# Optimization experiments

Hardware: AMD Instinct MI355X
Metric: run time of the kernel (lower is better)

## Reference

```python
import jax, jax.numpy as jnp
import numpy as np

MU = 255.0
WINDOW, STRIDE = 16, 8
N_LAYERS, R = 16, 64
LOOP_FACTOR = 8  # floor(log2(max_dilation=128)) + 1


def mu_law_encode(x):
    x = jnp.clip(x, -1.0, 1.0)
    m = jnp.sign(x) * jnp.log1p(MU * jnp.abs(x)) / jnp.log1p(MU)
    return jnp.clip((m + 1.0) * 0.5 * MU + 0.5, 0, MU).astype(jnp.int32)


def conv_transpose1d(x, w, b, stride):
    # torch ConvTranspose1d semantics, weight [Cin, Cout, K], padding=0
    K = w.shape[-1]
    rhs = jnp.transpose(jnp.flip(w, -1), (1, 0, 2))  # -> [Cout, Cin, K]
    y = jax.lax.conv_general_dilated(
        x, rhs, window_strides=(1,), padding=[(K - 1, K - 1)],
        lhs_dilation=(stride,), dimension_numbers=('NCH', 'OIH', 'NCH'))
    return y + b[None, :, None]


def causal_conv(x, w, b, dilation):
    # left-pad by (K-1)*dilation, then valid dilated conv (torch Conv1d weight [O,I,K])
    K = w.shape[-1]
    xp = jnp.pad(x, ((0, 0), (0, 0), ((K - 1) * dilation, 0)))
    y = jax.lax.conv_general_dilated(
        xp, w, window_strides=(1,), padding='VALID',
        rhs_dilation=(dilation,), dimension_numbers=('NCH', 'OIH', 'NCH'))
    return y + b[None, :, None]


def pconv(x, w, b=None):
    # 1x1 conv as matmul over channel dim
    y = jnp.einsum('oc,bct->bot', w, x)
    return y if b is None else y + b[None, :, None]


def wavenet_fwd(features, audio_q, w_up, b_up, w_cond, b_cond, embed,
                w_dil, b_dil, w_res, b_res, w_skip, b_skip, w_out, w_end):
    B, T = audio_q.shape
    cond = conv_transpose1d(features, w_up, b_up, STRIDE)
    pad = WINDOW - STRIDE  # fading == 'full'
    cond = cond[..., pad:-pad]
    cond = pconv(cond, w_cond, b_cond)        # applied inside get_cond_input
    cond = cond[..., :T]
    cond_acts = pconv(cond, w_cond, b_cond)   # applied AGAIN in forward (as in source)
    cond_acts = cond_acts.reshape(B, N_LAYERS, 2 * R, T)
    x = jnp.swapaxes(embed[audio_q], 1, 2)    # [B, R, T]
    output = None
    res_acts = None
    for i in range(N_LAYERS):
        d = 2 ** (i % LOOP_FACTOR)
        ia = causal_conv(x, w_dil[i], b_dil[i], d) + cond_acts[:, i]
        acts = jnp.tanh(ia[:, :R]) * jax.nn.sigmoid(ia[:, R:])
        if i < N_LAYERS - 1:
            res_acts = pconv(acts, w_res[i], b_res[i])
        x = res_acts + x  # last layer reuses previous res_acts (faithful to source)
        skip = pconv(acts, w_skip[i], b_skip[i])
        output = skip if i == 0 else output + skip
    out = jax.nn.relu(output)
    out = jax.nn.relu(pconv(out, w_out))      # conv_out, no bias
    out = pconv(out, w_end)                   # conv_end, no bias
    # shift right by one, first frame zeroed
    out = jnp.concatenate([jnp.zeros_like(out[:, :, :1]), out[:, :, :-1]], axis=2)
    return out


def setup_inputs() -> dict:
    key = jax.random.key(0)
    ks = jax.random.split(key, 16)
    f32 = jnp.float32
    return {
        'features': jax.random.normal(ks[0], (1, 2048, 128), f32),
        'audio': jax.random.uniform(ks[1], (1, 1016), f32, -1.0, 1.0),
        'w_up': jax.random.normal(ks[2], (2048, 2048, 16), f32) * 0.01,
        'b_up': jax.random.normal(ks[3], (2048,), f32) * 0.01,
        'w_cond': jax.random.normal(ks[4], (2048, 2048), f32) * 0.02,
        'b_cond': jax.random.normal(ks[5], (2048,), f32) * 0.02,
        'embed': jax.random.normal(ks[6], (256, 64), f32) * 0.1,
        'w_dil': jax.random.normal(ks[7], (16, 128, 64, 2), f32) * 0.1,
        'b_dil': jax.random.normal(ks[8], (16, 128), f32) * 0.02,
        'w_res': jax.random.normal(ks[9], (15, 64, 64), f32) * 0.1,
        'b_res': jax.random.normal(ks[10], (15, 64), f32) * 0.02,
        'w_skip': jax.random.normal(ks[11], (16, 256, 64), f32) * 0.1,
        'b_skip': jax.random.normal(ks[12], (16, 256), f32) * 0.02,
        'w_out': jax.random.normal(ks[13], (256, 256), f32) * 0.05,
        'w_end': jax.random.normal(ks[14], (256, 256), f32) * 0.05,
    }


def reference(features, audio, w_up, b_up, w_cond, b_cond, embed,
              w_dil, b_dil, w_res, b_res, w_skip, b_skip, w_out, w_end):
    q = mu_law_encode(audio)
    out = wavenet_fwd(features, q, w_up, b_up, w_cond, b_cond, embed,
                      w_dil, b_dil, w_res, b_res, w_skip, b_skip, w_out, w_end)
    return (out, q)
```

## Files before the change

kernel.cpp:

```cpp
#include <hip/hip_runtime.h>
#include <math.h>

#define T_LEN 1016

typedef __attribute__((ext_vector_type(8))) short bf16x8;
typedef __attribute__((ext_vector_type(4))) float f32x4;
typedef __attribute__((ext_vector_type(4))) unsigned int uint4v;
typedef __attribute__((ext_vector_type(2))) unsigned int uint2v;

static __device__ __forceinline__ unsigned pk_bf16(float lo, float hi) {
    unsigned r;
    asm("v_cvt_pk_bf16_f32 %0, %1, %2" : "=v"(r) : "v"(lo), "v"(hi));
    return r;
}

#define F4C(v, i) ((i) == 0 ? (v).x : (i) == 1 ? (v).y : (i) == 2 ? (v).z : (v).w)

__global__ void k_mulaw_embed(const float* __restrict__ audio,
                              const float* __restrict__ embed,
                              float* __restrict__ x0,
                              float* __restrict__ q_out)
{
    int t = blockIdx.x * blockDim.x + threadIdx.x;
    if (t >= T_LEN) return;
    float x = audio[t];
    x = fminf(1.f, fmaxf(-1.f, x));
    float ax = fabsf(x);
    float sg = (x > 0.f) ? 1.f : ((x < 0.f) ? -1.f : 0.f);
    float m = sg * log1pf(255.f * ax) / log1pf(255.f);
    float v = (m + 1.f) * 0.5f * 255.f + 0.5f;
    v = fminf(255.f, fmaxf(0.f, v));
    int q = (int)v;
    q_out[t] = (float)q;
    const float* e = embed + q * 64;
    for (int c = 0; c < 64; ++c) x0[(size_t)c * T_LEN + t] = e[c];
}

__global__ __launch_bounds__(256) void k_cvt_bf16(const float* __restrict__ src,
                                                  unsigned short* __restrict__ dst)
{
    int i4 = (blockIdx.x * 256 + threadIdx.x) * 4;
    float4 v = *(const float4*)&src[i4];
    uint2v p;
    p.x = pk_bf16(v.x, v.y);
    p.y = pk_bf16(v.z, v.w);
    *(uint2v*)&dst[i4] = p;
}

__global__ __launch_bounds__(256) void k_build_f2t(const float* __restrict__ F,
                                                   unsigned short* __restrict__ f2t)
{
    int oct = blockIdx.x;
    for (int c = threadIdx.x; c < 2048; c += 256) {
        float v0 = (oct < 127) ? F[(size_t)c * 128 + oct] : 0.f;
        float v1 = (oct < 127) ? F[(size_t)c * 128 + oct + 1] : 0.f;
        *(unsigned*)&f2t[(size_t)oct * 4096 + 2 * c] = pk_bf16(v0, v1);
    }
}

__global__ __launch_bounds__(256) void k_upsample_mfma(
    const unsigned short* __restrict__ f2t,
    const float* __restrict__ W,
    const float* __restrict__ b_up,
    unsigned short* __restrict__ cond0)
{
    __shared__ char lds_raw[49152];

    const int tid  = threadIdx.x;
    const int wave = tid >> 6;
    const int lane = tid & 63;
    const int ob   = blockIdx.x * 8;
    const int wm = wave & 1, wn = wave >> 1;
    const int row = lane & 15, g = lane >> 4;

    int cj[2], wbyte[2][4];
    size_t aWoff[2];
    #pragma unroll
    for (int j = 0; j < 2; ++j) {
        int flat = j * 256 + tid;
        int cp = flat >> 4;
        int op = (flat >> 1) & 7;
        int h  = flat & 1;
        cj[j] = cp;
        aWoff[j] = (size_t)cp * 32768 + (size_t)(ob + op) * 16 + h * 4;
        #pragma unroll
        for (int i = 0; i < 4; ++i) {
            int ph = h * 4 + i;
            int m  = op * 8 + ph;
            wbyte[j][i] = m * 128 + ((cp * 4) ^ (ph << 4));
        }
    }
    const int bn = tid >> 1, bhalf = tid & 1;
    int bSrc[4], bbw[4];
    #pragma unroll
    for (int q = 0; q < 4; ++q) {
        bSrc[q] = bn * 4096 + bhalf * 32 + q * 8;
        bbw[q]  = bn * 128 + ((((bhalf * 4 + q) * 16)) ^ ((bn & 7) << 4));
    }
    int abyte[2][2], bbyte[2][4];
    #pragma unroll
    for (int s = 0; s < 2; ++s) {
        #pragma unroll
        for (int fm = 0; fm < 2; ++fm) {
            int m = wm * 32 + fm * 16 + row;
            abyte[s][fm] = m * 128 + (((s * 4 + g) * 16) ^ ((m & 7) << 4));
        }
        #pragma unroll
        for (int fn = 0; fn < 4; ++fn) {
            int n = wn * 64 + fn * 16 + row;
            bbyte[s][fn] = n * 128 + (((s * 4 + g) * 16) ^ ((n & 7) << 4));
        }
    }

    f32x4 acc[2][4];
    #pragma unroll
    for (int a = 0; a < 2; ++a)
        #pragma unroll
        for (int b = 0; b < 4; ++b) acc[a][b] = (f32x4){0.f, 0.f, 0.f, 0.f};

    float4 aL[2], aH[2];
    uint4v bstg[4];

    #pragma unroll
    for (int j = 0; j < 2; ++j) {
        const float* p = W + aWoff[j];
        aL[j] = *(const float4*)p;
        aH[j] = *(const float4*)(p + 8);
    }
    #pragma unroll
    for (int q = 0; q < 4; ++q)
        bstg[q] = *(const uint4v*)(f2t + bSrc[q]);
    #pragma unroll
    for (int j = 0; j < 2; ++j)
        #pragma unroll
        for (int i = 0; i < 4; ++i)
            *(unsigned*)(lds_raw + wbyte[j][i]) = pk_bf16(F4C(aH[j], i), F4C(aL[j], i));
    #pragma unroll
    for (int q = 0; q < 4; ++q)
        *(uint4v*)(lds_raw + 16384 + bbw[q]) = bstg[q];
    __syncthreads();

    int cur = 0;
    for (int r = 0; r < 64; ++r) {
        const bool more = (r < 63);
        if (more) {
            const size_t roff = (size_t)(r + 1) * (32 * 32768);
            #pragma unroll
            for (int j = 0; j < 2; ++j) {
                const float* p = W + aWoff[j] + roff;
                aL[j] = *(const float4*)p;
                aH[j] = *(const float4*)(p + 8);
            }
            const int bo = (r + 1) * 64;
            #pragma unroll
            for (int q = 0; q < 4; ++q)
                bstg[q] = *(const uint4v*)(f2t + bSrc[q] + bo);
        }
        {
            const char* As = lds_raw + cur * 8192;
            const char* Bs = lds_raw + 16384 + cur * 16384;
            #pragma unroll
            for (int s = 0; s < 2; ++s) {
                bf16x8 af[2];
                #pragma unroll
                for (int fm = 0; fm < 2; ++fm)
                    af[fm] = *(const bf16x8*)(As + abyte[s][fm]);
                #pragma unroll
                for (int fn = 0; fn < 4; ++fn) {
                    bf16x8 bf = *(const bf16x8*)(Bs + bbyte[s][fn]);
                    acc[0][fn] = __builtin_amdgcn_mfma_f32_16x16x32_bf16(af[0], bf, acc[0][fn], 0, 0, 0);
                    acc[1][fn] = __builtin_amdgcn_mfma_f32_16x16x32_bf16(af[1], bf, acc[1][fn], 0, 0, 0);
                }
            }
        }
        if (more) {
            char* As = lds_raw + (cur ^ 1) * 8192;
            char* Bs = lds_raw + 16384 + (cur ^ 1) * 16384;
            #pragma unroll
            for (int j = 0; j < 2; ++j)
                #pragma unroll
                for (int i = 0; i < 4; ++i)
                    *(unsigned*)(As + wbyte[j][i]) = pk_bf16(F4C(aH[j], i), F4C(aL[j], i));
            #pragma unroll
            for (int q = 0; q < 4; ++q)
                *(uint4v*)(Bs + bbw[q]) = bstg[q];
        }
        __syncthreads();
        cur ^= 1;
    }

    #pragma unroll
    for (int fm = 0; fm < 2; ++fm) {
        const int och = ob + wm * 4 + fm * 2 + (g >> 1);
        const int ph0 = (g & 1) * 4;
        const float bb = b_up[och];
        #pragma unroll
        for (int fn = 0; fn < 4; ++fn) {
            const int oct = wn * 64 + fn * 16 + row;
            if (oct == 127) continue;
            float v0 = acc[fm][fn].x + bb;
            float v1 = acc[fm][fn].y + bb;
            float v2 = acc[fm][fn].z + bb;
            float v3 = acc[fm][fn].w + bb;
            uint2v pkd;
            pkd.x = pk_bf16(v0, v1);
            pkd.y = pk_bf16(v2, v3);
            *(uint2v*)&cond0[(size_t)och * 1024 + oct * 8 + ph0] = pkd;
        }
    }
}

__global__ __launch_bounds__(256) void k_transpose_bf16(const unsigned short* __restrict__ src,
                                                        unsigned short* __restrict__ dst)
{
    __shared__ unsigned short sm[64][68];
    const int t0 = blockIdx.x * 64, o0 = blockIdx.y * 64;
    const int tid = threadIdx.x;
    const int r = tid >> 4;
    const int c4 = (tid & 15) * 4;
    #pragma unroll
    for (int p = 0; p < 4; ++p) {
        int o = p * 16 + r;
        ushort4 v = *(const ushort4*)(src + (size_t)(o0 + o) * 1024 + t0 + c4);
        sm[o][c4 + 0] = v.x; sm[o][c4 + 1] = v.y;
        sm[o][c4 + 2] = v.z; sm[o][c4 + 3] = v.w;
    }
    __syncthreads();
    #pragma unroll
    for (int p = 0; p < 4; ++p) {
        int t = p * 16 + r;
        int tg = t0 + t;
        ushort4 v;
        if (tg < 1016) {
            v.x = sm[c4 + 0][t]; v.y = sm[c4 + 1][t];
            v.z = sm[c4 + 2][t]; v.w = sm[c4 + 3][t];
        } else {
            v.x = 0; v.y = 0; v.z = 0; v.w = 0;
        }
        *(ushort4*)(dst + (size_t)tg * 2048 + o0 + c4) = v;
    }
}

template<int MODE>
__global__ __launch_bounds__(256) void gemm_mfma(
    const unsigned short* __restrict__ A, const unsigned short* __restrict__ Bm,
    const float* __restrict__ bias, void* __restrict__ outp,
    int ldA, int ldB, int K)
{
    const int w = threadIdx.x >> 6, lane = threadIdx.x & 63;
    const int m0 = blockIdx.y * 128 + (w >> 1) * 64;
    const int n0 = blockIdx.x * 128 + (w & 1) * 64;
    const int row = lane & 15, g = lane >> 4;

    f32x4 acc[4][4];
    #pragma unroll
    for (int i = 0; i < 4; ++i)
        #pragma unroll
        for (int j = 0; j < 4; ++j) acc[i][j] = (f32x4){0.f, 0.f, 0.f, 0.f};

    const unsigned short* Ap = A + (size_t)(m0 + row) * ldA + g * 8;
    const unsigned short* Bp = Bm + (size_t)(n0 + row) * ldB + g * 8;

    for (int kk = 0; kk < K; kk += 32) {
        bf16x8 af[4], bf[4];
        #pragma unroll
        for (int fm = 0; fm < 4; ++fm)
            af[fm] = *(const bf16x8*)(Ap + (size_t)fm * 16 * ldA + kk);
        #pragma unroll
        for (int fn = 0; fn < 4; ++fn)
            bf[fn] = *(const bf16x8*)(Bp + (size_t)fn * 16 * ldB + kk);
        #pragma unroll
        for (int fm = 0; fm < 4; ++fm)
            #pragma unroll
            for (int fn = 0; fn < 4; ++fn)
                acc[fm][fn] = __builtin_amdgcn_mfma_f32_16x16x32_bf16(af[fm], bf[fn], acc[fm][fn], 0, 0, 0);
    }

    #pragma unroll
    for (int fm = 0; fm < 4; ++fm) {
        #pragma unroll
        for (int fn = 0; fn < 4; ++fn) {
            const int n_g = n0 + fn * 16 + row;
            const int m_b = m0 + fm * 16 + g * 4;
            if (MODE == 0) {
                unsigned short* o = (unsigned short*)outp;
                const float bb = bias[n_g];
                #pragma unroll
                for (int r = 0; r < 4; ++r) {
                    float v = F4C(acc[fm][fn], r) + bb;
                    o[(size_t)(m_b + r) * 2048 + n_g] = (unsigned short)pk_bf16(v, v);
                }
            } else {
                float* o = (float*)outp;
                if (n_g < 1016) {
                    #pragma unroll
                    for (int r = 0; r < 4; ++r) {
                        float v = F4C(acc[fm][fn], r) + bias[m_b + r];
                        o[(size_t)(m_b + r) * 1016 + n_g] = v;
                    }
                }
            }
        }
    }
}

template<bool RELU_IN, bool RELU_OUT, bool SHIFT>
__global__ __launch_bounds__(256) void gemm_f32(
    const float* __restrict__ W, const float* __restrict__ X,
    const float* __restrict__ bias, float* __restrict__ Y,
    int M, int K, int N)
{
    __shared__ float ws_s[16][68];
    __shared__ float xs_s[16][68];
    const int m0 = blockIdx.y * 64;
    const int n0 = blockIdx.x * 64;
    const int tid = threadIdx.x;
    const int tx = tid & 15, ty = tid >> 4;

    float acc[4][4];
    #pragma unroll
    for (int i = 0; i < 4; ++i)
        #pragma unroll
        for (int j = 0; j < 4; ++j) acc[i][j] = 0.f;

    for (int kk = 0; kk < K; kk += 16) {
        {
            int m = tid >> 2;
            int k4 = (tid & 3) * 4;
            float4 v = *(const float4*)&W[(size_t)(m0 + m) * K + kk + k4];
            ws_s[k4 + 0][m] = v.x; ws_s[k4 + 1][m] = v.y;
            ws_s[k4 + 2][m] = v.z; ws_s[k4 + 3][m] = v.w;
        }
        {
            int k = tid >> 4;
            int n4 = (tid & 15) * 4;
            int n = n0 + n4;
            float4 v;
            if (n + 3 < N) v = *(const float4*)&X[(size_t)(kk + k) * N + n];
            else {
                v.x = (n + 0 < N) ? X[(size_t)(kk + k) * N + n + 0] : 0.f;
                v.y = (n + 1 < N) ? X[(size_t)(kk + k) * N + n + 1] : 0.f;
                v.z = (n + 2 < N) ? X[(size_t)(kk + k) * N + n + 2] : 0.f;
                v.w = (n + 3 < N) ? X[(size_t)(kk + k) * N + n + 3] : 0.f;
            }
            if (RELU_IN) {
                v.x = fmaxf(v.x, 0.f); v.y = fmaxf(v.y, 0.f);
                v.z = fmaxf(v.z, 0.f); v.w = fmaxf(v.w, 0.f);
            }
            *(float4*)&xs_s[k][n4] = v;
        }
        __syncthreads();
        #pragma unroll
        for (int k = 0; k < 16; ++k) {
            float a[4], b[4];
            #pragma unroll
            for (int i = 0; i < 4; ++i) a[i] = ws_s[k][ty * 4 + i];
            #pragma unroll
            for (int j = 0; j < 4; ++j) b[j] = xs_s[k][tx * 4 + j];
            #pragma unroll
            for (int i = 0; i < 4; ++i)
                #pragma unroll
                for (int j = 0; j < 4; ++j) acc[i][j] += a[i] * b[j];
        }
        __syncthreads();
    }
    #pragma unroll
    for (int i = 0; i < 4; ++i) {
        int m = m0 + ty * 4 + i;
        float bb = bias ? bias[m] : 0.f;
        #pragma unroll
        for (int j = 0; j < 4; ++j) {
            int n = n0 + tx * 4 + j;
            float v = acc[i][j] + bb;
            if (RELU_OUT) v = fmaxf(v, 0.f);
            if (!SHIFT) {
                if (n < N) Y[(size_t)m * N + n] = v;
            } else {
                if (n == 0) Y[(size_t)m * N] = 0.f;
                if (n + 1 < N) Y[(size_t)m * N + n + 1] = v;
            }
        }
    }
}

__global__ __launch_bounds__(256) void k_layer(
    const float* __restrict__ x_in,
    float* __restrict__ x_out,
    const float* __restrict__ cond,
    const float* __restrict__ w_dil,
    const float* __restrict__ b_dil,
    const float* __restrict__ w_res,
    const float* __restrict__ b_res,
    const float* __restrict__ w_skip,
    const float* __restrict__ b_skip,
    float* __restrict__ skip_acc,
    int d, int first, int last)
{
    __shared__ float xs[64 * 136];
    __shared__ float ia_s[128 * 9];
    __shared__ float acts_s[64 * 9];
    const int tid = threadIdx.x;
    const int t0 = blockIdx.x * 8;
    const int w = 8 + d;

    int count = 64 * w;
    for (int idx = tid; idx < count; idx += 256) {
        int c = idx / w, tt = idx - c * w;
        int tg = t0 - d + tt;
        xs[idx] = (tg >= 0) ? x_in[(size_t)c * T_LEN + tg] : 0.f;
    }
    __syncthreads();

    {
        int o = tid & 127;
        int tq = tid >> 7;
        float ia[4];
        #pragma unroll
        for (int s = 0; s < 4; ++s) {
            int t = tq + 2 * s;
            ia[s] = b_dil[o] + cond[(size_t)o * T_LEN + t0 + t];
        }
        const float* wd = w_dil + (size_t)o * 128;
        for (int c = 0; c < 64; ++c) {
            float w0 = wd[c * 2], w1 = wd[c * 2 + 1];
            const float* xr = xs + c * w;
            #pragma unroll
            for (int s = 0; s < 4; ++s) {
                int t = tq + 2 * s;
                ia[s] += w0 * xr[t] + w1 * xr[t + d];
            }
        }
        #pragma unroll
        for (int s = 0; s < 4; ++s) {
            int t = tq + 2 * s;
            ia_s[o * 9 + t] = ia[s];
        }
    }
    __syncthreads();

    #pragma unroll
    for (int rep = 0; rep < 2; ++rep) {
        int idx = tid + rep * 256;
        int c = idx >> 3, t = idx & 7;
        float a = ia_s[c * 9 + t];
        float gg = ia_s[(c + 64) * 9 + t];
        acts_s[c * 9 + t] = tanhf(a) * (1.f / (1.f + expf(-gg)));
    }
    __syncthreads();

    {
        int o = tid;
        float acc[8];
        #pragma unroll
        for (int t = 0; t < 8; ++t) acc[t] = 0.f;
        const float* wk = w_skip + (size_t)o * 64;
        for (int c = 0; c < 64; ++c) {
            float wv = wk[c];
            #pragma unroll
            for (int t = 0; t < 8; ++t) acc[t] += wv * acts_s[c * 9 + t];
        }
        float bb = b_skip[o];
        #pragma unroll
        for (int t = 0; t < 8; ++t) {
            size_t oidx = (size_t)o * T_LEN + t0 + t;
            float prev = first ? 0.f : skip_acc[oidx];
            skip_acc[oidx] = prev + acc[t] + bb;
        }
    }

    if (!last) {
        #pragma unroll
        for (int rep = 0; rep < 2; ++rep) {
            int idx = tid + rep * 256;
            int c = idx >> 3, t = idx & 7;
            float r = b_res[c];
            const float* wr = w_res + (size_t)c * 64;
            for (int cc = 0; cc < 64; ++cc) r += wr[cc] * acts_s[cc * 9 + t];
            x_out[(size_t)c * T_LEN + t0 + t] = r + xs[c * w + t + d];
        }
    }
}

extern "C" void kernel_launch(void* const* d_in, const int* in_sizes, int n_in,
                              void* d_out, int out_size, void* d_ws, size_t ws_size,
                              hipStream_t stream)
{
    const float* features = (const float*)d_in[0];
    const float* audio    = (const float*)d_in[1];
    const float* w_up     = (const float*)d_in[2];
    const float* b_up     = (const float*)d_in[3];
    const float* w_cond   = (const float*)d_in[4];
    const float* b_cond   = (const float*)d_in[5];
    const float* embed    = (const float*)d_in[6];
    const float* w_dil    = (const float*)d_in[7];
    const float* b_dil    = (const float*)d_in[8];
    const float* w_res    = (const float*)d_in[9];
    const float* b_res    = (const float*)d_in[10];
    const float* w_skip   = (const float*)d_in[11];
    const float* b_skip   = (const float*)d_in[12];
    const float* w_out    = (const float*)d_in[13];
    const float* w_end    = (const float*)d_in[14];
    float* out = (float*)d_out;

    char* base = (char*)d_ws;
    unsigned short* w_cond_b  = (unsigned short*)(base);
    unsigned short* f2t       = (unsigned short*)(base + 8388608);
    unsigned short* cond0     = (unsigned short*)(base + 9437184);
    unsigned short* cond0T    = (unsigned short*)(base + 13631488);
    unsigned short* condBT    = (unsigned short*)(base + 17825792);
    float*          cond_acts = (float*)(base + 22020096);
    float*          x0        = (float*)(base + 30343168);
    float*          x1        = (float*)(base + 30603264);
    float*          skip      = (float*)(base + 30863360);
    float*          h2        = (float*)(base + 31903744);

    k_mulaw_embed<<<4, 256, 0, stream>>>(audio, embed, x0, out + 260096);
    k_cvt_bf16<<<4096, 256, 0, stream>>>(w_cond, w_cond_b);
    k_build_f2t<<<128, 256, 0, stream>>>(features, f2t);
    k_upsample_mfma<<<256, 256, 0, stream>>>(f2t, w_up, b_up, cond0);
    k_transpose_bf16<<<dim3(16, 32), 256, 0, stream>>>(cond0, cond0T);
    gemm_mfma<0><<<dim3(16, 8), 256, 0, stream>>>(cond0T, w_cond_b, b_cond, condBT, 2048, 2048, 2048);
    gemm_mfma<1><<<dim3(8, 16), 256, 0, stream>>>(w_cond_b, condBT, b_cond, cond_acts, 2048, 2048, 2048);

    float* xbuf[2] = {x0, x1};
    for (int i = 0; i < 16; ++i) {
        int d = 1 << (i & 7);
        k_layer<<<127, 256, 0, stream>>>(
            xbuf[i & 1], xbuf[(i + 1) & 1],
            cond_acts + (size_t)i * 128 * T_LEN,
            w_dil + (size_t)i * 16384, b_dil + i * 128,
            (i < 15) ? (w_res + (size_t)i * 4096) : (const float*)nullptr,
            (i < 15) ? (b_res + i * 64) : (const float*)nullptr,
            w_skip + (size_t)i * 16384, b_skip + i * 256,
            skip, d, (i == 0) ? 1 : 0, (i == 15) ? 1 : 0);
    }

    gemm_f32<true, true, false><<<dim3(16, 4), 256, 0, stream>>>(
        w_out, skip, nullptr, h2, 256, 256, T_LEN);
    gemm_f32<false, false, true><<<dim3(16, 4), 256, 0, stream>>>(
        w_end, h2, nullptr, out, 256, 256, T_LEN);
}
```

Baseline: 1.009 ms.

## Fuse WaveNet layer chain and output head into one persistent kernel with flag sync

Replaces the sixteen per-layer launches and the two output GEMM launches with one persistent kernel of 127 blocks. Each block owns an 8-sample time tile, keeps skip accumulators in registers, and waits on per-block progress flags for only the predecessor tiles its dilation reaches. Each layer's output is written to a separate global buffer so later blocks can read it. The output head (relu, w_out, relu, w_end) is fused into the tail, and the feature-transpose kernel now stages through LDS with coalesced float4 loads. This removes launch gaps and skip-buffer round trips, but it relies on all 127 blocks being co-resident and adds spin-wait latency along the dependency chain.

```diff
diff --git a/kernel.cpp b/kernel.cpp
--- a/kernel.cpp
+++ b/kernel.cpp
@@ -2,6 +2,7 @@
 #include <math.h>
 
 #define T_LEN 1016
+#define XSTRIDE 65024
 
 typedef __attribute__((ext_vector_type(8))) short bf16x8;
 typedef __attribute__((ext_vector_type(4))) float f32x4;
@@ -50,12 +51,25 @@
 __global__ __launch_bounds__(256) void k_build_f2t(const float* __restrict__ F,
                                                    unsigned short* __restrict__ f2t)
 {
-    int oct = blockIdx.x;
-    for (int c = threadIdx.x; c < 2048; c += 256) {
-        float v0 = (oct < 127) ? F[(size_t)c * 128 + oct] : 0.f;
-        float v1 = (oct < 127) ? F[(size_t)c * 128 + oct + 1] : 0.f;
-        *(unsigned*)&f2t[(size_t)oct * 4096 + 2 * c] = pk_bf16(v0, v1);
-    }
+    __shared__ float fs[32][129];
+    const int tid = threadIdx.x;
+    const int c0 = blockIdx.x * 32;
+    #pragma unroll
+    for (int p = 0; p < 4; ++p) {
+        int idx = p * 256 + tid;
+        int cl = idx >> 5;
+        int o4 = (idx & 31) * 4;
+        float4 v = *(const float4*)&F[(size_t)(c0 + cl) * 128 + o4];
+        fs[cl][o4 + 0] = v.x; fs[cl][o4 + 1] = v.y;
+        fs[cl][o4 + 2] = v.z; fs[cl][o4 + 3] = v.w;
+    }
+    __syncthreads();
+    for (int idx = tid; idx < 127 * 32; idx += 256) {
+        int oct = idx >> 5, cc = idx & 31;
+        *(unsigned*)&f2t[(size_t)oct * 4096 + 2 * (c0 + cc)] = pk_bf16(fs[cc][oct], fs[cc][oct + 1]);
+    }
+    if (tid < 32)
+        *(unsigned*)&f2t[(size_t)127 * 4096 + 2 * (c0 + tid)] = 0u;
 }
 
 __global__ __launch_bounds__(256) void k_upsample_mfma(
@@ -73,7 +87,7 @@
     const int wm = wave & 1, wn = wave >> 1;
     const int row = lane & 15, g = lane >> 4;
 
-    int cj[2], wbyte[2][4];
+    int wbyte[2][4];
     size_t aWoff[2];
     #pragma unroll
     for (int j = 0; j < 2; ++j) {
@@ -81,7 +95,6 @@
         int cp = flat >> 4;
         int op = (flat >> 1) & 7;
         int h  = flat & 1;
-        cj[j] = cp;
         aWoff[j] = (size_t)cp * 32768 + (size_t)(ob + op) * 16 + h * 4;
         #pragma unroll
         for (int i = 0; i < 4; ++i) {
@@ -304,180 +317,192 @@
     }
 }
 
-template<bool RELU_IN, bool RELU_OUT, bool SHIFT>
-__global__ __launch_bounds__(256) void gemm_f32(
-    const float* __restrict__ W, const float* __restrict__ X,
-    const float* __restrict__ bias, float* __restrict__ Y,
-    int M, int K, int N)
-{
-    __shared__ float ws_s[16][68];
-    __shared__ float xs_s[16][68];
-    const int m0 = blockIdx.y * 64;
-    const int n0 = blockIdx.x * 64;
+__global__ __launch_bounds__(256) void k_chain(
+    const float* __restrict__ x0,
+    float* __restrict__ xch,
+    const float* __restrict__ cond_acts,
+    const float* __restrict__ w_dil, const float* __restrict__ b_dil,
+    const float* __restrict__ w_res, const float* __restrict__ b_res,
+    const float* __restrict__ w_skip, const float* __restrict__ b_skip,
+    const float* __restrict__ w_out, const float* __restrict__ w_end,
+    float* __restrict__ out,
+    int* __restrict__ prog)
+{
+    __shared__ float xsA[64 * 8];
+    __shared__ float xow[64 * 8];
+    __shared__ float ia_s[128 * 9];
+    __shared__ float acts_s[64 * 8];
+    __shared__ float h1_s[256 * 8];
+    __shared__ float h2_s[256 * 8];
+
     const int tid = threadIdx.x;
-    const int tx = tid & 15, ty = tid >> 4;
-
-    float acc[4][4];
-    #pragma unroll
-    for (int i = 0; i < 4; ++i)
-        #pragma unroll
-        for (int j = 0; j < 4; ++j) acc[i][j] = 0.f;
-
-    for (int kk = 0; kk < K; kk += 16) {
+    const int b = blockIdx.x;
+    const int t0 = b * 8;
+
+    #pragma unroll
+    for (int r = 0; r < 2; ++r) {
+        int idx = tid + r * 256;
+        int c = idx >> 3, t = idx & 7;
+        xow[c * 8 + (t & 1) * 4 + (t >> 1)] = x0[c * T_LEN + t0 + t];
+    }
+    float skip_r[8] = {0.f, 0.f, 0.f, 0.f, 0.f, 0.f, 0.f, 0.f};
+
+    for (int i = 0; i < 16; ++i) {
+        const int d = 1 << (i & 7);
+        const float* xin = (i == 0) ? x0 : (xch + (size_t)(i - 1) * XSTRIDE);
+
+        if (i > 0) {
+            int K = (d + 7) >> 3;
+            int nb = (K < b) ? K : b;
+            if (tid < nb) {
+                const int* fl = prog + (b - 1 - tid) * 16;
+                while (__hip_atomic_load(fl, __ATOMIC_RELAXED, __HIP_MEMORY_SCOPE_AGENT) < i)
+                    __builtin_amdgcn_s_sleep(2);
+            }
+            __syncthreads();
+            __threadfence();
+        }
+        #pragma unroll
+        for (int r = 0; r < 2; ++r) {
+            int idx = tid + r * 256;
+            int c = idx >> 3, t = idx & 7;
+            int tg = t0 - d + t;
+            xsA[c * 8 + (t & 1) * 4 + (t >> 1)] = (tg >= 0) ? xin[c * T_LEN + tg] : 0.f;
+        }
+        __syncthreads();
+
         {
-            int m = tid >> 2;
-            int k4 = (tid & 3) * 4;
-            float4 v = *(const float4*)&W[(size_t)(m0 + m) * K + kk + k4];
-            ws_s[k4 + 0][m] = v.x; ws_s[k4 + 1][m] = v.y;
-            ws_s[k4 + 2][m] = v.z; ws_s[k4 + 3][m] = v.w;
-        }
-        {
-            int k = tid >> 4;
-            int n4 = (tid & 15) * 4;
-            int n = n0 + n4;
-            float4 v;
-            if (n + 3 < N) v = *(const float4*)&X[(size_t)(kk + k) * N + n];
-            else {
-                v.x = (n + 0 < N) ? X[(size_t)(kk + k) * N + n + 0] : 0.f;
-                v.y = (n + 1 < N) ? X[(size_t)(kk + k) * N + n + 1] : 0.f;
-                v.z = (n + 2 < N) ? X[(size_t)(kk + k) * N + n + 2] : 0.f;
-                v.w = (n + 3 < N) ? X[(size_t)(kk + k) * N + n + 3] : 0.f;
-            }
-            if (RELU_IN) {
-                v.x = fmaxf(v.x, 0.f); v.y = fmaxf(v.y, 0.f);
-                v.z = fmaxf(v.z, 0.f); v.w = fmaxf(v.w, 0.f);
-            }
-            *(float4*)&xs_s[k][n4] = v;
+            const int o = tid & 127, tq = tid >> 7;
+            const float* cd = cond_acts + ((size_t)i * 128 + o) * T_LEN + t0;
+            float ia[4];
+            #pragma unroll
+            for (int s2 = 0; s2 < 4; ++s2) ia[s2] = b_dil[i * 128 + o] + cd[tq + 2 * s2];
+            const float* wd = w_dil + (size_t)i * 16384 + o * 128;
+            for (int c = 0; c < 64; ++c) {
+                float2 wv = *(const float2*)&wd[2 * c];
+                float4 xa = *(const float4*)&xsA[c * 8 + tq * 4];
+                float4 xo = *(const float4*)&xow[c * 8 + tq * 4];
+                ia[0] += wv.x * xa.x + wv.y * xo.x;
+                ia[1] += wv.x * xa.y + wv.y * xo.y;
+                ia[2] += wv.x * xa.z + wv.y * xo.z;
+                ia[3] += wv.x * xa.w + wv.y * xo.w;
+            }
+            #pragma unroll
+            for (int s2 = 0; s2 < 4; ++s2) ia_s[o * 9 + tq + 2 * s2] = ia[s2];
         }
         __syncthreads();
-        #pragma unroll
-        for (int k = 0; k < 16; ++k) {
-            float a[4], b[4];
-            #pragma unroll
-            for (int i = 0; i < 4; ++i) a[i] = ws_s[k][ty * 4 + i];
-            #pragma unroll
-            for (int j = 0; j < 4; ++j) b[j] = xs_s[k][tx * 4 + j];
-            #pragma unroll
-            for (int i = 0; i < 4; ++i)
-                #pragma unroll
-                for (int j = 0; j < 4; ++j) acc[i][j] += a[i] * b[j];
-        }
-        __syncthreads();
-    }
-    #pragma unroll
-    for (int i = 0; i < 4; ++i) {
-        int m = m0 + ty * 4 + i;
-        float bb = bias ? bias[m] : 0.f;
-        #pragma unroll
-        for (int j = 0; j < 4; ++j) {
-            int n = n0 + tx * 4 + j;
-            float v = acc[i][j] + bb;
-            if (RELU_OUT) v = fmaxf(v, 0.f);
-            if (!SHIFT) {
-                if (n < N) Y[(size_t)m * N + n] = v;
-            } else {
-                if (n == 0) Y[(size_t)m * N] = 0.f;
-                if (n + 1 < N) Y[(size_t)m * N + n + 1] = v;
-            }
-        }
-    }
-}
-
-__global__ __launch_bounds__(256) void k_layer(
-    const float* __restrict__ x_in,
-    float* __restrict__ x_out,
-    const float* __restrict__ cond,
-    const float* __restrict__ w_dil,
-    const float* __restrict__ b_dil,
-    const float* __restrict__ w_res,
-    const float* __restrict__ b_res,
-    const float* __restrict__ w_skip,
-    const float* __restrict__ b_skip,
-    float* __restrict__ skip_acc,
-    int d, int first, int last)
-{
-    __shared__ float xs[64 * 136];
-    __shared__ float ia_s[128 * 9];
-    __shared__ float acts_s[64 * 9];
-    const int tid = threadIdx.x;
-    const int t0 = blockIdx.x * 8;
-    const int w = 8 + d;
-
-    int count = 64 * w;
-    for (int idx = tid; idx < count; idx += 256) {
-        int c = idx / w, tt = idx - c * w;
-        int tg = t0 - d + tt;
-        xs[idx] = (tg >= 0) ? x_in[(size_t)c * T_LEN + tg] : 0.f;
-    }
-    __syncthreads();
-
-    {
-        int o = tid & 127;
-        int tq = tid >> 7;
-        float ia[4];
-        #pragma unroll
-        for (int s = 0; s < 4; ++s) {
-            int t = tq + 2 * s;
-            ia[s] = b_dil[o] + cond[(size_t)o * T_LEN + t0 + t];
-        }
-        const float* wd = w_dil + (size_t)o * 128;
-        for (int c = 0; c < 64; ++c) {
-            float w0 = wd[c * 2], w1 = wd[c * 2 + 1];
-            const float* xr = xs + c * w;
-            #pragma unroll
-            for (int s = 0; s < 4; ++s) {
-                int t = tq + 2 * s;
-                ia[s] += w0 * xr[t] + w1 * xr[t + d];
-            }
-        }
-        #pragma unroll
-        for (int s = 0; s < 4; ++s) {
-            int t = tq + 2 * s;
-            ia_s[o * 9 + t] = ia[s];
-        }
-    }
-    __syncthreads();
-
-    #pragma unroll
-    for (int rep = 0; rep < 2; ++rep) {
-        int idx = tid + rep * 256;
-        int c = idx >> 3, t = idx & 7;
-        float a = ia_s[c * 9 + t];
-        float gg = ia_s[(c + 64) * 9 + t];
-        acts_s[c * 9 + t] = tanhf(a) * (1.f / (1.f + expf(-gg)));
-    }
-    __syncthreads();
-
-    {
-        int o = tid;
-        float acc[8];
-        #pragma unroll
-        for (int t = 0; t < 8; ++t) acc[t] = 0.f;
-        const float* wk = w_skip + (size_t)o * 64;
-        for (int c = 0; c < 64; ++c) {
-            float wv = wk[c];
-            #pragma unroll
-            for (int t = 0; t < 8; ++t) acc[t] += wv * acts_s[c * 9 + t];
-        }
-        float bb = b_skip[o];
-        #pragma unroll
-        for (int t = 0; t < 8; ++t) {
-            size_t oidx = (size_t)o * T_LEN + t0 + t;
-            float prev = first ? 0.f : skip_acc[oidx];
-            skip_acc[oidx] = prev + acc[t] + bb;
-        }
-    }
-
-    if (!last) {
+
         #pragma unroll
         for (int rep = 0; rep < 2; ++rep) {
             int idx = tid + rep * 256;
             int c = idx >> 3, t = idx & 7;
-            float r = b_res[c];
-            const float* wr = w_res + (size_t)c * 64;
-            for (int cc = 0; cc < 64; ++cc) r += wr[cc] * acts_s[cc * 9 + t];
-            x_out[(size_t)c * T_LEN + t0 + t] = r + xs[c * w + t + d];
-        }
+            float a = ia_s[c * 9 + t];
+            float gg = ia_s[(c + 64) * 9 + t];
+            acts_s[c * 8 + t] = tanhf(a) * (1.f / (1.f + expf(-gg)));
+        }
+        __syncthreads();
+
+        {
+            const float* wk = w_skip + (size_t)i * 16384 + tid * 64;
+            float acc[8] = {0.f, 0.f, 0.f, 0.f, 0.f, 0.f, 0.f, 0.f};
+            for (int c4 = 0; c4 < 16; ++c4) {
+                float4 wv = *(const float4*)&wk[c4 * 4];
+                #pragma unroll
+                for (int u = 0; u < 4; ++u) {
+                    float w1 = F4C(wv, u);
+                    float4 a0 = *(const float4*)&acts_s[(c4 * 4 + u) * 8];
+                    float4 a1 = *(const float4*)&acts_s[(c4 * 4 + u) * 8 + 4];
+                    acc[0] += w1 * a0.x; acc[1] += w1 * a0.y;
+                    acc[2] += w1 * a0.z; acc[3] += w1 * a0.w;
+                    acc[4] += w1 * a1.x; acc[5] += w1 * a1.y;
+                    acc[6] += w1 * a1.z; acc[7] += w1 * a1.w;
+                }
+            }
+            float bb = b_skip[i * 256 + tid];
+            #pragma unroll
+            for (int t = 0; t < 8; ++t) skip_r[t] += acc[t] + bb;
+        }
+
+        if (i < 15) {
+            float* xo_g = xch + (size_t)i * XSTRIDE;
+            #pragma unroll
+            for (int rep = 0; rep < 2; ++rep) {
+                int idx = tid + rep * 256;
+                int c = idx >> 3, t = idx & 7;
+                float r = b_res[i * 64 + c];
+                const float* wr = w_res + (size_t)i * 4096 + c * 64;
+                for (int cc = 0; cc < 64; ++cc) r += wr[cc] * acts_s[cc * 8 + t];
+                int xoff = c * 8 + (t & 1) * 4 + (t >> 1);
+                r += xow[xoff];
+                xow[xoff] = r;
+                xo_g[c * T_LEN + t0 + t] = r;
+            }
+            __syncthreads();
+            __threadfence();
+            if (tid == 0)
+                __hip_atomic_store(prog + b * 16, i + 1, __ATOMIC_RELEASE, __HIP_MEMORY_SCOPE_AGENT);
+        } else {
+            __syncthreads();
+        }
+    }
+
+    {
+        float4 lo, hi;
+        lo.x = fmaxf(skip_r[0], 0.f); lo.y = fmaxf(skip_r[1], 0.f);
+        lo.z = fmaxf(skip_r[2], 0.f); lo.w = fmaxf(skip_r[3], 0.f);
+        hi.x = fmaxf(skip_r[4], 0.f); hi.y = fmaxf(skip_r[5], 0.f);
+        hi.z = fmaxf(skip_r[6], 0.f); hi.w = fmaxf(skip_r[7], 0.f);
+        *(float4*)&h1_s[tid * 8] = lo;
+        *(float4*)&h1_s[tid * 8 + 4] = hi;
+    }
+    __syncthreads();
+    {
+        const float* wo = w_out + tid * 256;
+        float acc[8] = {0.f, 0.f, 0.f, 0.f, 0.f, 0.f, 0.f, 0.f};
+        for (int o4 = 0; o4 < 64; ++o4) {
+            float4 wv = *(const float4*)&wo[o4 * 4];
+            #pragma unroll
+            for (int u = 0; u < 4; ++u) {
+                float w1 = F4C(wv, u);
+                float4 a0 = *(const float4*)&h1_s[(o4 * 4 + u) * 8];
+                float4 a1 = *(const float4*)&h1_s[(o4 * 4 + u) * 8 + 4];
+                acc[0] += w1 * a0.x; acc[1] += w1 * a0.y;
+                acc[2] += w1 * a0.z; acc[3] += w1 * a0.w;
+                acc[4] += w1 * a1.x; acc[5] += w1 * a1.y;
+                acc[6] += w1 * a1.z; acc[7] += w1 * a1.w;
+            }
+        }
+        float4 lo, hi;
+        lo.x = fmaxf(acc[0], 0.f); lo.y = fmaxf(acc[1], 0.f);
+        lo.z = fmaxf(acc[2], 0.f); lo.w = fmaxf(acc[3], 0.f);
+        hi.x = fmaxf(acc[4], 0.f); hi.y = fmaxf(acc[5], 0.f);
+        hi.z = fmaxf(acc[6], 0.f); hi.w = fmaxf(acc[7], 0.f);
+        *(float4*)&h2_s[tid * 8] = lo;
+        *(float4*)&h2_s[tid * 8 + 4] = hi;
+    }
+    __syncthreads();
+    {
+        const float* we = w_end + tid * 256;
+        float acc[8] = {0.f, 0.f, 0.f, 0.f, 0.f, 0.f, 0.f, 0.f};
+        for (int m4 = 0; m4 < 64; ++m4) {
+            float4 wv = *(const float4*)&we[m4 * 4];
+            #pragma unroll
+            for (int u = 0; u < 4; ++u) {
+                float w1 = F4C(wv, u);
+                float4 a0 = *(const float4*)&h2_s[(m4 * 4 + u) * 8];
+                float4 a1 = *(const float4*)&h2_s[(m4 * 4 + u) * 8 + 4];
+                acc[0] += w1 * a0.x; acc[1] += w1 * a0.y;
+                acc[2] += w1 * a0.z; acc[3] += w1 * a0.w;
+                acc[4] += w1 * a1.x; acc[5] += w1 * a1.y;
+                acc[6] += w1 * a1.z; acc[7] += w1 * a1.w;
+            }
+        }
+        #pragma unroll
+        for (int t = 0; t < 8; ++t) {
+            int tg = t0 + 1 + t;
+            if (tg < T_LEN) out[tid * T_LEN + tg] = acc[t];
+        }
+        if (b == 0) out[tid * T_LEN] = 0.f;
     }
 }
 
@@ -510,33 +535,18 @@
     unsigned short* condBT    = (unsigned short*)(base + 17825792);
     float*          cond_acts = (float*)(base + 22020096);
     float*          x0        = (float*)(base + 30343168);
-    float*          x1        = (float*)(base + 30603264);
-    float*          skip      = (float*)(base + 30863360);
-    float*          h2        = (float*)(base + 31903744);
-
+    float*          xch       = (float*)(base + 30603264);
+    int*            prog      = (int*)(base + 34764800);
+
+    hipMemsetAsync(prog, 0, 8192, stream);
     k_mulaw_embed<<<4, 256, 0, stream>>>(audio, embed, x0, out + 260096);
     k_cvt_bf16<<<4096, 256, 0, stream>>>(w_cond, w_cond_b);
-    k_build_f2t<<<128, 256, 0, stream>>>(features, f2t);
+    k_build_f2t<<<64, 256, 0, stream>>>(features, f2t);
     k_upsample_mfma<<<256, 256, 0, stream>>>(f2t, w_up, b_up, cond0);
     k_transpose_bf16<<<dim3(16, 32), 256, 0, stream>>>(cond0, cond0T);
     gemm_mfma<0><<<dim3(16, 8), 256, 0, stream>>>(cond0T, w_cond_b, b_cond, condBT, 2048, 2048, 2048);
     gemm_mfma<1><<<dim3(8, 16), 256, 0, stream>>>(w_cond_b, condBT, b_cond, cond_acts, 2048, 2048, 2048);
-
-    float* xbuf[2] = {x0, x1};
-    for (int i = 0; i < 16; ++i) {
-        int d = 1 << (i & 7);
-        k_layer<<<127, 256, 0, stream>>>(
-            xbuf[i & 1], xbuf[(i + 1) & 1],
-            cond_acts + (size_t)i * 128 * T_LEN,
-            w_dil + (size_t)i * 16384, b_dil + i * 128,
-            (i < 15) ? (w_res + (size_t)i * 4096) : (const float*)nullptr,
-            (i < 15) ? (b_res + i * 64) : (const float*)nullptr,
-            w_skip + (size_t)i * 16384, b_skip + i * 256,
-            skip, d, (i == 0) ? 1 : 0, (i == 15) ? 1 : 0);
-    }
-
-    gemm_f32<true, true, false><<<dim3(16, 4), 256, 0, stream>>>(
-        w_out, skip, nullptr, h2, 256, 256, T_LEN);
-    gemm_f32<false, false, true><<<dim3(16, 4), 256, 0, stream>>>(
-        w_end, h2, nullptr, out, 256, 256, T_LEN);
-}
+    k_chain<<<127, 256, 0, stream>>>(x0, xch, cond_acts,
+                                     w_dil, b_dil, w_res, b_res, w_skip, b_skip,
+                                     w_out, w_end, out, prog);
+}
```

New measurement: 1.366 ms. 35.3% more time.
